# Kernel tuning notes

Hardware: AMD Instinct MI355X
Metric: run time of the kernel (lower is better)

Reference implementation:

```python
import jax, jax.numpy as jnp
import numpy as np

B, L, E, H = 2, 2048, 2048, 16
HD = E // H  # 128
ROPE_BASE = 10000.0


def setup_inputs() -> dict:
    key = jax.random.key(0)
    k1, k2, k3 = jax.random.split(key, 3)
    x = jax.random.normal(k1, (B, L, E), dtype=jnp.float32)
    position_ids = jnp.tile(jnp.arange(L, dtype=jnp.int32)[None, :], (B, 1))
    # Linear weights stored as [in, out] so y = x @ W + b (equals torch x @ W.T + b)
    W_attn = jax.random.normal(k2, (E, 3 * E), dtype=jnp.float32) * (1.0 / np.sqrt(E))
    b_attn = jnp.zeros((3 * E,), dtype=jnp.float32)
    W_proj = jax.random.normal(k3, (E, E), dtype=jnp.float32) * (1.0 / np.sqrt(E))
    b_proj = jnp.zeros((E,), dtype=jnp.float32)
    return {"x": x, "position_ids": position_ids, "W_attn": W_attn,
            "b_attn": b_attn, "W_proj": W_proj, "b_proj": b_proj}


def _rotate_half(t):
    h = t.shape[-1] // 2
    return jnp.concatenate([-t[..., h:], t[..., :h]], axis=-1)


def _apply_rope(q, k, position_ids):
    # q,k: [B,H,L,HD]; position_ids: [B,L]
    inv_freq = 1.0 / (ROPE_BASE ** (jnp.arange(0, HD, 2, dtype=jnp.float32) / HD))
    angles = position_ids.astype(jnp.float32)[:, :, None] * inv_freq  # [B,L,HD/2]
    cos = jnp.concatenate([jnp.cos(angles)] * 2, axis=-1)[:, None]  # [B,1,L,HD]
    sin = jnp.concatenate([jnp.sin(angles)] * 2, axis=-1)[:, None]
    return q * cos + _rotate_half(q) * sin, k * cos + _rotate_half(k) * sin


def reference(x, position_ids, W_attn, b_attn, W_proj, b_proj):
    # fused QKV projection
    qkv = x @ W_attn + b_attn                       # [B,L,3E]
    q, k, v = jnp.split(qkv, 3, axis=-1)            # each [B,L,E]
    reshape = lambda t: t.reshape(B, L, H, HD).transpose(0, 2, 1, 3)  # [B,H,L,HD]
    q, k, v = reshape(q), reshape(k), reshape(v)
    q, k = _apply_rope(q, k, position_ids)
    # scaled dot-product attention (mask=None -> full attention, dropout 0)
    scores = jnp.einsum('bhqd,bhkd->bhqk', q, k) * (1.0 / np.sqrt(HD))
    probs = jax.nn.softmax(scores, axis=-1)
    y = jnp.einsum('bhqk,bhkd->bhqd', probs, v)     # [B,H,L,HD]
    y = y.transpose(0, 2, 1, 3).reshape(B, L, E)
    return y @ W_proj + b_proj
```

## Files before the change

kernel.cpp:

```cpp
#include <hip/hip_runtime.h>
#include <math.h>

#define BB 2
#define LL 2048
#define EE 2048
#define HH 16
#define HD 128
#define N3E (3*EE)

typedef __attribute__((ext_vector_type(8))) short  bf16x8;
typedef __attribute__((ext_vector_type(4))) float  f32x4;

__device__ __forceinline__ ushort f2bf(float f) {
    union { float f; unsigned u; } v; v.f = f;
    unsigned u = v.u + 0x7FFFu + ((v.u >> 16) & 1u);
    return (ushort)(u >> 16);
}
__device__ __forceinline__ float bf2f(ushort u) {
    union { unsigned u; float f; } v; v.u = ((unsigned)u) << 16;
    return v.f;
}

#define NB_CVT 4096
#define NB_T1  12288
#define NB_T2  4096

__device__ __forceinline__ void tr_block(const float* __restrict__ in,
                                         ushort* __restrict__ out,
                                         int R, int Ccol, int bx, int by,
                                         float (*tile)[33], int t) {
    int c0 = bx * 32, r0 = by * 32;
    int lr = t >> 5, lc = t & 31;
    #pragma unroll
    for (int i = 0; i < 4; ++i)
        tile[lr + i * 8][lc] = in[(size_t)(r0 + lr + i * 8) * Ccol + c0 + lc];
    __syncthreads();
    #pragma unroll
    for (int i = 0; i < 4; ++i)
        out[(size_t)(c0 + lr + i * 8) * R + r0 + lc] = f2bf(tile[lc][lr + i * 8]);
}

__global__ __launch_bounds__(256) void pre_all(const float* __restrict__ x,
                                               ushort* __restrict__ xb,
                                               const float* __restrict__ W_attn,
                                               ushort* __restrict__ Wat,
                                               const float* __restrict__ W_proj,
                                               ushort* __restrict__ Wpt) {
    __shared__ float tile[32][33];
    int bid = blockIdx.x;
    int t = threadIdx.x;
    if (bid < NB_CVT) {
        int i = (bid * 256 + t) * 8;
        float4 a = *(const float4*)(x + i);
        float4 b = *(const float4*)(x + i + 4);
        ushort4 p0 = { f2bf(a.x), f2bf(a.y), f2bf(a.z), f2bf(a.w) };
        ushort4 p1 = { f2bf(b.x), f2bf(b.y), f2bf(b.z), f2bf(b.w) };
        *(ushort4*)(xb + i)     = p0;
        *(ushort4*)(xb + i + 4) = p1;
    } else if (bid < NB_CVT + NB_T1) {
        int lb = bid - NB_CVT;
        tr_block(W_attn, Wat, EE, N3E, lb % (N3E / 32), lb / (N3E / 32), tile, t);
    } else {
        int lb = bid - NB_CVT - NB_T1;
        tr_block(W_proj, Wpt, EE, EE, lb % (EE / 32), lb / (EE / 32), tile, t);
    }
}

template<int WRITE_BF16>
__global__ __launch_bounds__(512, 2) void gemm_ktile(const ushort* __restrict__ A,
                                                     const ushort* __restrict__ Bt,
                                                     const float* __restrict__ bias,
                                                     void* __restrict__ C,
                                                     int M, int N, int K, int nbx) {
    __shared__ __align__(16) ushort Asl[4 * 8192];
    __shared__ __align__(16) ushort Bsl[4 * 4096];

    const int t    = threadIdx.x;
    const int lane = t & 63;
    const int w    = t >> 6;
    const int m    = lane & 15;
    const int quad = lane >> 4;
    const int wm   = w >> 1;
    const int wn   = w & 1;

    const int nwg = gridDim.x;
    const int cpx = nwg >> 3;
    const int swz = ((int)blockIdx.x & 7) * cpx + ((int)blockIdx.x >> 3);
    const int bx  = swz % nbx;
    const int by  = swz / nbx;
    const int m0  = by * 256, n0 = bx * 128;

    const int r16s  = (t >> 2) & 15;
    const int kels  = ((t & 3) ^ ((t & 32) ? 2 : 0)) * 8;
    const int row0s = ((t >> 6) << 4) + r16s;
    const int row1s = row0s + 128;

    const int foff = m * 32 + ((quad * 8) ^ ((m & 8) ? 16 : 0));

#define STAGE(T_) do { int _s = (T_) & 3; \
    __builtin_amdgcn_global_load_lds( \
        (const __attribute__((address_space(1))) unsigned int*)(A + (size_t)(m0 + row0s) * K + (T_) * 32 + kels), \
        (__attribute__((address_space(3))) unsigned int*)(Asl + _s * 8192 + t * 8), 16, 0, 0); \
    __builtin_amdgcn_global_load_lds( \
        (const __attribute__((address_space(1))) unsigned int*)(A + (size_t)(m0 + row1s) * K + (T_) * 32 + kels), \
        (__attribute__((address_space(3))) unsigned int*)(Asl + _s * 8192 + (512 + t) * 8), 16, 0, 0); \
    __builtin_amdgcn_global_load_lds( \
        (const __attribute__((address_space(1))) unsigned int*)(Bt + (size_t)(n0 + row0s) * K + (T_) * 32 + kels), \
        (__attribute__((address_space(3))) unsigned int*)(Bsl + _s * 4096 + t * 8), 16, 0, 0); } while (0)

    f32x4 acc[4][4];
    #pragma unroll
    for (int i = 0; i < 4; ++i)
        #pragma unroll
        for (int j = 0; j < 4; ++j) acc[i][j] = (f32x4){0.f, 0.f, 0.f, 0.f};

    const int NT = K >> 5;

    STAGE(0); STAGE(1); STAGE(2);
    asm volatile("s_waitcnt vmcnt(6)" ::: "memory");
    __builtin_amdgcn_s_barrier();

    for (int T = 0; T < NT; ++T) {
        const int slot = T & 3;
        const ushort* as = Asl + slot * 8192 + wm * 2048;
        const ushort* bs = Bsl + slot * 4096 + wn * 2048;

        bf16x8 af[4], bf[4];
        #pragma unroll
        for (int mt = 0; mt < 4; ++mt)
            af[mt] = *(const bf16x8*)(as + mt * 512 + foff);
        #pragma unroll
        for (int nt = 0; nt < 4; ++nt)
            bf[nt] = *(const bf16x8*)(bs + nt * 512 + foff);

        if (T + 3 < NT) STAGE(T + 3);

        if (T + 3 < NT)      asm volatile("s_waitcnt vmcnt(6)" ::: "memory");
        else if (T + 2 < NT) asm volatile("s_waitcnt vmcnt(3)" ::: "memory");
        else                 asm volatile("s_waitcnt vmcnt(0)" ::: "memory");
        __builtin_amdgcn_s_barrier();
        asm volatile("s_waitcnt lgkmcnt(0)" ::: "memory");
        __builtin_amdgcn_s_setprio(1);
        #pragma unroll
        for (int mt = 0; mt < 4; ++mt)
            #pragma unroll
            for (int nt = 0; nt < 4; ++nt)
                acc[mt][nt] = __builtin_amdgcn_mfma_f32_16x16x32_bf16(af[mt], bf[nt], acc[mt][nt], 0, 0, 0);
        __builtin_amdgcn_s_setprio(0);
        __builtin_amdgcn_s_barrier();
    }
#undef STAGE

    float bcol[4];
    #pragma unroll
    for (int nt = 0; nt < 4; ++nt) bcol[nt] = bias[n0 + wn * 64 + nt * 16 + m];
    #pragma unroll
    for (int mt = 0; mt < 4; ++mt) {
        #pragma unroll
        for (int nt = 0; nt < 4; ++nt) {
            #pragma unroll
            for (int r = 0; r < 4; ++r) {
                int row = m0 + wm * 64 + mt * 16 + quad * 4 + r;
                int col = n0 + wn * 64 + nt * 16 + m;
                float v = acc[mt][nt][r] + bcol[nt];
                if (WRITE_BF16) ((ushort*)C)[(size_t)row * N + col] = f2bf(v);
                else            ((float*)C)[(size_t)row * N + col] = v;
            }
        }
    }
}

__global__ __launch_bounds__(256) void prep_qkv(const ushort* __restrict__ qkvb,
                                                const int* __restrict__ pos_ids,
                                                ushort* __restrict__ Qt,
                                                ushort* __restrict__ Kt,
                                                ushort* __restrict__ Vtt) {
    __shared__ ushort vlds[64 * 136];
    int bid = blockIdx.x;
    int t   = threadIdx.x;

    if (bid < 4096) {
        const float scale = 0.08838834764831845f;
        const float nl2b = -0.20762050593046014f;
        int idx = bid * 256 + t;
        int p    = idx & 15;
        int r    = (idx >> 4) & 63;
        int tile = (idx >> 10) & 31;
        int h    = (idx >> 15) & 15;
        int b    = idx >> 19;
        int c    = p ^ (r & 15);
        int l    = tile * 64 + r;
        int half = c >> 3, cl = c & 7;
        const ushort* row = qkvb + (size_t)(b * LL + l) * N3E;
        float pos = (float)pos_ids[b * LL + l];

        bf16x8 qa = *(const bf16x8*)(row + h * HD + c * 8);
        bf16x8 qb = *(const bf16x8*)(row + h * HD + (c ^ 8) * 8);
        bf16x8 ka = *(const bf16x8*)(row + EE + h * HD + c * 8);
        bf16x8 kb = *(const bf16x8*)(row + EE + h * HD + (c ^ 8) * 8);
        bf16x8 qo, ko;
        #pragma unroll
        for (int i = 0; i < 8; ++i) {
            int j = cl * 8 + i;
            float ang = pos * exp2f((float)j * nl2b);
            float s, cs;
            sincosf(ang, &s, &cs);
            float sgn = half ? s : -s;
            float q1 = bf2f((ushort)qa[i]), q2 = bf2f((ushort)qb[i]);
            float k1 = bf2f((ushort)ka[i]), k2 = bf2f((ushort)kb[i]);
            qo[i] = (short)f2bf((q1 * cs + q2 * sgn) * scale);
            ko[i] = (short)f2bf(k1 * cs + k2 * sgn);
        }
        size_t obase = ((size_t)(b * 16 + h) * 32 + tile) * 8192 + r * 128 + p * 8;
        *(bf16x8*)(Qt + obase) = qo;
        *(bf16x8*)(Kt + obase) = ko;
    } else {
        int vb   = bid - 4096;
        int tile = vb & 31;
        int bh   = vb >> 5;
        int b    = bh >> 4, h = bh & 15;

        #pragma unroll
        for (int it = 0; it < 4; ++it) {
            int c4 = t + it * 256;
            int kk = c4 >> 4, dc = c4 & 15;
            bf16x8 v = *(const bf16x8*)(qkvb + (size_t)(b * LL + tile * 64 + kk) * N3E
                                        + 2 * EE + h * HD + dc * 8);
            int colp = (dc * 8) ^ ((kk >> 3) << 4);
            *(bf16x8*)(vlds + kk * 136 + colp) = v;
        }
        __syncthreads();
        #pragma unroll
        for (int it = 0; it < 4; ++it) {
            int oc = t + it * 256;
            int p = oc & 7, r = oc >> 3;
            int c = p ^ (r & 7);
            bf16x8 o;
            #pragma unroll
            for (int i = 0; i < 8; ++i) {
                int kk = c * 8 + i;
                o[i] = (short)vlds[kk * 136 + (r ^ ((kk >> 3) << 4))];
            }
            *(bf16x8*)(Vtt + ((size_t)bh * 32 + tile) * 8192 + r * 64 + p * 8) = o;
        }
    }
}

#define PSTR 68

__global__ __launch_bounds__(256, 2) void flash2(const ushort* __restrict__ Qt,
                                                 const ushort* __restrict__ Kt,
                                                 const ushort* __restrict__ Vtt,
                                                 ushort* __restrict__ y) {
    __shared__ __align__(16) ushort Ks[64 * 128];
    __shared__ __align__(16) ushort Vs[128 * 64];
    __shared__ __align__(16) ushort Ps[4 * 32 * PSTR];

    const int t    = threadIdx.x;
    const int w    = t >> 6;
    const int lane = t & 63;
    const int m    = lane & 15;
    const int quad = lane >> 4;
    const int qblk = blockIdx.x;
    const int bh   = blockIdx.y;
    const int b    = bh >> 4, h = bh & 15;

    const ushort* Qhead = Qt  + (size_t)bh * 32 * 8192;
    const ushort* Khead = Kt  + (size_t)bh * 32 * 8192;
    const ushort* Vhead = Vtt + (size_t)bh * 32 * 8192;

    bf16x8 qf[2][4];
    #pragma unroll
    for (int mt = 0; mt < 2; ++mt) {
        int rloc = w * 32 + mt * 16 + m;
        const ushort* qtile = Qhead + (size_t)(qblk * 2 + (rloc >> 6)) * 8192
                              + (rloc & 63) * 128;
        #pragma unroll
        for (int ks = 0; ks < 4; ++ks)
            qf[mt][ks] = *(const bf16x8*)(qtile + ((ks * 4 + quad) ^ m) * 8);
    }

    f32x4 oacc[2][8];
    #pragma unroll
    for (int mt = 0; mt < 2; ++mt)
        #pragma unroll
        for (int dt = 0; dt < 8; ++dt) oacc[mt][dt] = (f32x4){0.f, 0.f, 0.f, 0.f};
    float m_i[8], l_pl[8];
    #pragma unroll
    for (int s = 0; s < 8; ++s) { m_i[s] = -INFINITY; l_pl[s] = 0.f; }

    {
        const ushort* ksrc = Khead;
        #pragma unroll
        for (int i = 0; i < 4; ++i) {
            int cid = t + i * 256;
            __builtin_amdgcn_global_load_lds(
                (const __attribute__((address_space(1))) unsigned int*)(ksrc + cid * 8),
                (__attribute__((address_space(3))) unsigned int*)(Ks + cid * 8),
                16, 0, 0);
        }
    }

    for (int kt = 0; kt < 32; ++kt) {
        asm volatile("s_waitcnt vmcnt(0)\n\ts_barrier" ::: "memory");

        {
            const ushort* vsrc = Vhead + (size_t)kt * 8192;
            #pragma unroll
            for (int i = 0; i < 4; ++i) {
                int cid = t + i * 256;
                __builtin_amdgcn_global_load_lds(
                    (const __attribute__((address_space(1))) unsigned int*)(vsrc + cid * 8),
                    (__attribute__((address_space(3))) unsigned int*)(Vs + cid * 8),
                    16, 0, 0);
            }
        }

        f32x4 sacc[2][4];
        #pragma unroll
        for (int mt = 0; mt < 2; ++mt)
            #pragma unroll
            for (int nt = 0; nt < 4; ++nt) sacc[mt][nt] = (f32x4){0.f, 0.f, 0.f, 0.f};
        __builtin_amdgcn_s_setprio(1);
        #pragma unroll
        for (int ks = 0; ks < 4; ++ks) {
            #pragma unroll
            for (int nt = 0; nt < 4; ++nt) {
                bf16x8 kf = *(const bf16x8*)&Ks[(nt * 16 + m) * 128 + (((ks * 4 + quad) ^ m)) * 8];
                sacc[0][nt] = __builtin_amdgcn_mfma_f32_16x16x32_bf16(qf[0][ks], kf, sacc[0][nt], 0, 0, 0);
                sacc[1][nt] = __builtin_amdgcn_mfma_f32_16x16x32_bf16(qf[1][ks], kf, sacc[1][nt], 0, 0, 0);
            }
        }
        __builtin_amdgcn_s_setprio(0);

        float mxs[2][4];
        #pragma unroll
        for (int mt = 0; mt < 2; ++mt) {
            #pragma unroll
            for (int r = 0; r < 4; ++r) {
                float mx = fmaxf(fmaxf(sacc[mt][0][r], sacc[mt][1][r]),
                                 fmaxf(sacc[mt][2][r], sacc[mt][3][r]));
                #pragma unroll
                for (int off = 1; off < 16; off <<= 1) mx = fmaxf(mx, __shfl_xor(mx, off, 64));
                mxs[mt][r] = mx;
            }
        }
        int small = 1;
        #pragma unroll
        for (int mt = 0; mt < 2; ++mt)
            #pragma unroll
            for (int r = 0; r < 4; ++r)
                small &= (mxs[mt][r] <= m_i[mt * 4 + r] + 8.0f) ? 1 : 0;

        if (__all(small)) {
            #pragma unroll
            for (int mt = 0; mt < 2; ++mt) {
                #pragma unroll
                for (int r = 0; r < 4; ++r) {
                    int slot = mt * 4 + r;
                    float mnew = m_i[slot];
                    float rs = 0.f;
                    #pragma unroll
                    for (int nt = 0; nt < 4; ++nt) {
                        float pv = __expf(sacc[mt][nt][r] - mnew);
                        sacc[mt][nt][r] = pv;
                        rs += pv;
                    }
                    l_pl[slot] += rs;
                }
            }
        } else {
            float alpha_s[2][4];
            #pragma unroll
            for (int mt = 0; mt < 2; ++mt) {
                #pragma unroll
                for (int r = 0; r < 4; ++r) {
                    int slot = mt * 4 + r;
                    float mnew = fmaxf(m_i[slot], mxs[mt][r]);
                    float al = __expf(m_i[slot] - mnew);
                    m_i[slot] = mnew;
                    float rs = 0.f;
                    #pragma unroll
                    for (int nt = 0; nt < 4; ++nt) {
                        float pv = __expf(sacc[mt][nt][r] - mnew);
                        sacc[mt][nt][r] = pv;
                        rs += pv;
                    }
                    l_pl[slot] = l_pl[slot] * al + rs;
                    alpha_s[mt][r] = al;
                }
            }
            #pragma unroll
            for (int mt = 0; mt < 2; ++mt)
                #pragma unroll
                for (int dt = 0; dt < 8; ++dt)
                    #pragma unroll
                    for (int r = 0; r < 4; ++r) oacc[mt][dt][r] *= alpha_s[mt][r];
        }

        #pragma unroll
        for (int mt = 0; mt < 2; ++mt)
            #pragma unroll
            for (int nt = 0; nt < 4; ++nt)
                #pragma unroll
                for (int r = 0; r < 4; ++r)
                    Ps[w * 32 * PSTR + (mt * 16 + quad * 4 + r) * PSTR + nt * 16 + m]
                        = f2bf(sacc[mt][nt][r]);

        asm volatile("s_waitcnt vmcnt(0)\n\ts_barrier" ::: "memory");

        if (kt + 1 < 32) {
            const ushort* ksrc = Khead + (size_t)(kt + 1) * 8192;
            #pragma unroll
            for (int i = 0; i < 4; ++i) {
                int cid = t + i * 256;
                __builtin_amdgcn_global_load_lds(
                    (const __attribute__((address_space(1))) unsigned int*)(ksrc + cid * 8),
                    (__attribute__((address_space(3))) unsigned int*)(Ks + cid * 8),
                    16, 0, 0);
            }
        }

        __builtin_amdgcn_s_setprio(1);
        #pragma unroll
        for (int ks2 = 0; ks2 < 2; ++ks2) {
            bf16x8 pf0 = *(const bf16x8*)&Ps[w * 32 * PSTR + (0 * 16 + m) * PSTR + ks2 * 32 + quad * 8];
            bf16x8 pf1 = *(const bf16x8*)&Ps[w * 32 * PSTR + (1 * 16 + m) * PSTR + ks2 * 32 + quad * 8];
            #pragma unroll
            for (int dt = 0; dt < 8; ++dt) {
                bf16x8 vf = *(const bf16x8*)&Vs[(dt * 16 + m) * 64 + (((ks2 * 4 + quad) ^ (m & 7))) * 8];
                oacc[0][dt] = __builtin_amdgcn_mfma_f32_16x16x32_bf16(pf0, vf, oacc[0][dt], 0, 0, 0);
                oacc[1][dt] = __builtin_amdgcn_mfma_f32_16x16x32_bf16(pf1, vf, oacc[1][dt], 0, 0, 0);
            }
        }
        __builtin_amdgcn_s_setprio(0);
    }

    #pragma unroll
    for (int s = 0; s < 8; ++s) {
        #pragma unroll
        for (int off = 1; off < 16; off <<= 1) l_pl[s] += __shfl_xor(l_pl[s], off, 64);
        l_pl[s] = 1.0f / l_pl[s];
    }
    #pragma unroll
    for (int mt = 0; mt < 2; ++mt) {
        #pragma unroll
        for (int dt = 0; dt < 8; ++dt) {
            #pragma unroll
            for (int r = 0; r < 4; ++r) {
                int row = qblk * 128 + w * 32 + mt * 16 + quad * 4 + r;
                y[(size_t)(b * LL + row) * EE + h * HD + dt * 16 + m]
                    = f2bf(oacc[mt][dt][r] * l_pl[mt * 4 + r]);
            }
        }
    }
}

extern "C" void kernel_launch(void* const* d_in, const int* in_sizes, int n_in,
                              void* d_out, int out_size, void* d_ws, size_t ws_size,
                              hipStream_t stream) {
    const float* x      = (const float*)d_in[0];
    const int*   pos    = (const int*)d_in[1];
    const float* W_attn = (const float*)d_in[2];
    const float* b_attn = (const float*)d_in[3];
    const float* W_proj = (const float*)d_in[4];
    const float* b_proj = (const float*)d_in[5];
    float* out = (float*)d_out;

    const int M = BB * LL;
    ushort* xb   = (ushort*)d_ws;
    ushort* Wat  = xb   + (size_t)M * EE;
    ushort* Wpt  = Wat  + (size_t)N3E * EE;
    ushort* qkvb = Wpt  + (size_t)EE * EE;
    ushort* Kt   = qkvb + (size_t)M * N3E;
    ushort* Vtt  = Kt   + (size_t)M * EE;
    ushort* Qt   = xb;
    ushort* yb   = Wat;

    pre_all<<<dim3(NB_CVT + NB_T1 + NB_T2), dim3(256), 0, stream>>>(
        x, xb, W_attn, Wat, W_proj, Wpt);

    gemm_ktile<1><<<dim3((M / 256) * (N3E / 128)), dim3(512), 0, stream>>>(
        xb, Wat, b_attn, qkvb, M, N3E, EE, N3E / 128);

    prep_qkv<<<dim3(4096 + 1024), dim3(256), 0, stream>>>(qkvb, pos, Qt, Kt, Vtt);

    flash2<<<dim3(LL / 128, BB * HH), dim3(256), 0, stream>>>(Qt, Kt, Vtt, yb);

    gemm_ktile<0><<<dim3((M / 256) * (EE / 128)), dim3(512), 0, stream>>>(
        yb, Wpt, b_proj, out, M, EE, EE, EE / 128);
}
```

Measured before the change: 467.1 us.

## Read K/V fragments directly from global memory instead of staging through LDS

After: 453.9 us. 2.8% less time.

```diff
diff --git a/kernel.cpp b/kernel.cpp
--- a/kernel.cpp
+++ b/kernel.cpp
@@ -252,8 +252,6 @@
                                                  const ushort* __restrict__ Kt,
                                                  const ushort* __restrict__ Vtt,
                                                  ushort* __restrict__ y) {
-    __shared__ __align__(16) ushort Ks[64 * 128];
-    __shared__ __align__(16) ushort Vs[128 * 64];
     __shared__ __align__(16) ushort Ps[4 * 32 * PSTR];
 
     const int t    = threadIdx.x;
@@ -289,114 +287,56 @@
     #pragma unroll
     for (int s = 0; s < 8; ++s) { m_i[s] = -INFINITY; l_pl[s] = 0.f; }
 
-    {
-        const ushort* ksrc = Khead;
-        #pragma unroll
-        for (int i = 0; i < 4; ++i) {
-            int cid = t + i * 256;
-            __builtin_amdgcn_global_load_lds(
-                (const __attribute__((address_space(1))) unsigned int*)(ksrc + cid * 8),
-                (__attribute__((address_space(3))) unsigned int*)(Ks + cid * 8),
-                16, 0, 0);
-        }
-    }
-
     for (int kt = 0; kt < 32; ++kt) {
-        asm volatile("s_waitcnt vmcnt(0)\n\ts_barrier" ::: "memory");
-
-        {
-            const ushort* vsrc = Vhead + (size_t)kt * 8192;
-            #pragma unroll
-            for (int i = 0; i < 4; ++i) {
-                int cid = t + i * 256;
-                __builtin_amdgcn_global_load_lds(
-                    (const __attribute__((address_space(1))) unsigned int*)(vsrc + cid * 8),
-                    (__attribute__((address_space(3))) unsigned int*)(Vs + cid * 8),
-                    16, 0, 0);
-            }
-        }
+        const ushort* ktile = Khead + (size_t)kt * 8192;
+        const ushort* vtile = Vhead + (size_t)kt * 8192;
 
         f32x4 sacc[2][4];
         #pragma unroll
         for (int mt = 0; mt < 2; ++mt)
             #pragma unroll
             for (int nt = 0; nt < 4; ++nt) sacc[mt][nt] = (f32x4){0.f, 0.f, 0.f, 0.f};
-        __builtin_amdgcn_s_setprio(1);
         #pragma unroll
         for (int ks = 0; ks < 4; ++ks) {
             #pragma unroll
             for (int nt = 0; nt < 4; ++nt) {
-                bf16x8 kf = *(const bf16x8*)&Ks[(nt * 16 + m) * 128 + (((ks * 4 + quad) ^ m)) * 8];
+                bf16x8 kf = *(const bf16x8*)(ktile + (nt * 16 + m) * 128
+                                             + (((ks * 4 + quad) ^ m)) * 8);
                 sacc[0][nt] = __builtin_amdgcn_mfma_f32_16x16x32_bf16(qf[0][ks], kf, sacc[0][nt], 0, 0, 0);
                 sacc[1][nt] = __builtin_amdgcn_mfma_f32_16x16x32_bf16(qf[1][ks], kf, sacc[1][nt], 0, 0, 0);
             }
         }
-        __builtin_amdgcn_s_setprio(0);
-
-        float mxs[2][4];
+
+        float alpha_s[2][4];
         #pragma unroll
         for (int mt = 0; mt < 2; ++mt) {
             #pragma unroll
             for (int r = 0; r < 4; ++r) {
+                int slot = mt * 4 + r;
                 float mx = fmaxf(fmaxf(sacc[mt][0][r], sacc[mt][1][r]),
                                  fmaxf(sacc[mt][2][r], sacc[mt][3][r]));
                 #pragma unroll
                 for (int off = 1; off < 16; off <<= 1) mx = fmaxf(mx, __shfl_xor(mx, off, 64));
-                mxs[mt][r] = mx;
-            }
-        }
-        int small = 1;
+                float mnew = fmaxf(m_i[slot], mx);
+                float al = __expf(m_i[slot] - mnew);
+                m_i[slot] = mnew;
+                float rs = 0.f;
+                #pragma unroll
+                for (int nt = 0; nt < 4; ++nt) {
+                    float pv = __expf(sacc[mt][nt][r] - mnew);
+                    sacc[mt][nt][r] = pv;
+                    rs += pv;
+                }
+                l_pl[slot] = l_pl[slot] * al + rs;
+                alpha_s[mt][r] = al;
+            }
+        }
         #pragma unroll
         for (int mt = 0; mt < 2; ++mt)
             #pragma unroll
-            for (int r = 0; r < 4; ++r)
-                small &= (mxs[mt][r] <= m_i[mt * 4 + r] + 8.0f) ? 1 : 0;
-
-        if (__all(small)) {
-            #pragma unroll
-            for (int mt = 0; mt < 2; ++mt) {
+            for (int dt = 0; dt < 8; ++dt)
                 #pragma unroll
-                for (int r = 0; r < 4; ++r) {
-                    int slot = mt * 4 + r;
-                    float mnew = m_i[slot];
-                    float rs = 0.f;
-                    #pragma unroll
-                    for (int nt = 0; nt < 4; ++nt) {
-                        float pv = __expf(sacc[mt][nt][r] - mnew);
-                        sacc[mt][nt][r] = pv;
-                        rs += pv;
-                    }
-                    l_pl[slot] += rs;
-                }
-            }
-        } else {
-            float alpha_s[2][4];
-            #pragma unroll
-            for (int mt = 0; mt < 2; ++mt) {
-                #pragma unroll
-                for (int r = 0; r < 4; ++r) {
-                    int slot = mt * 4 + r;
-                    float mnew = fmaxf(m_i[slot], mxs[mt][r]);
-                    float al = __expf(m_i[slot] - mnew);
-                    m_i[slot] = mnew;
-                    float rs = 0.f;
-                    #pragma unroll
-                    for (int nt = 0; nt < 4; ++nt) {
-                        float pv = __expf(sacc[mt][nt][r] - mnew);
-                        sacc[mt][nt][r] = pv;
-                        rs += pv;
-                    }
-                    l_pl[slot] = l_pl[slot] * al + rs;
-                    alpha_s[mt][r] = al;
-                }
-            }
-            #pragma unroll
-            for (int mt = 0; mt < 2; ++mt)
-                #pragma unroll
-                for (int dt = 0; dt < 8; ++dt)
-                    #pragma unroll
-                    for (int r = 0; r < 4; ++r) oacc[mt][dt][r] *= alpha_s[mt][r];
-        }
+                for (int r = 0; r < 4; ++r) oacc[mt][dt][r] *= alpha_s[mt][r];
 
         #pragma unroll
         for (int mt = 0; mt < 2; ++mt)
@@ -407,33 +347,18 @@
                     Ps[w * 32 * PSTR + (mt * 16 + quad * 4 + r) * PSTR + nt * 16 + m]
                         = f2bf(sacc[mt][nt][r]);
 
-        asm volatile("s_waitcnt vmcnt(0)\n\ts_barrier" ::: "memory");
-
-        if (kt + 1 < 32) {
-            const ushort* ksrc = Khead + (size_t)(kt + 1) * 8192;
-            #pragma unroll
-            for (int i = 0; i < 4; ++i) {
-                int cid = t + i * 256;
-                __builtin_amdgcn_global_load_lds(
-                    (const __attribute__((address_space(1))) unsigned int*)(ksrc + cid * 8),
-                    (__attribute__((address_space(3))) unsigned int*)(Ks + cid * 8),
-                    16, 0, 0);
-            }
-        }
-
-        __builtin_amdgcn_s_setprio(1);
         #pragma unroll
         for (int ks2 = 0; ks2 < 2; ++ks2) {
             bf16x8 pf0 = *(const bf16x8*)&Ps[w * 32 * PSTR + (0 * 16 + m) * PSTR + ks2 * 32 + quad * 8];
             bf16x8 pf1 = *(const bf16x8*)&Ps[w * 32 * PSTR + (1 * 16 + m) * PSTR + ks2 * 32 + quad * 8];
             #pragma unroll
             for (int dt = 0; dt < 8; ++dt) {
-                bf16x8 vf = *(const bf16x8*)&Vs[(dt * 16 + m) * 64 + (((ks2 * 4 + quad) ^ (m & 7))) * 8];
+                bf16x8 vf = *(const bf16x8*)(vtile + (dt * 16 + m) * 64
+                                             + (((ks2 * 4 + quad) ^ (m & 7))) * 8);
                 oacc[0][dt] = __builtin_amdgcn_mfma_f32_16x16x32_bf16(pf0, vf, oacc[0][dt], 0, 0, 0);
                 oacc[1][dt] = __builtin_amdgcn_mfma_f32_16x16x32_bf16(pf1, vf, oacc[1][dt], 0, 0, 0);
             }
         }
-        __builtin_amdgcn_s_setprio(0);
     }
 
     #pragma unroll
```
